# Optimization experiments

Measured on AMD Instinct MI355X. Metric: run time of the kernel, lower is better.

## Reference

```python
import math
import jax, jax.numpy as jnp
import numpy as np

NUM_EXPERTS = 64
HIDDEN = 2048
BATCH, SEQ = 8, 2048


def setup_inputs() -> dict:
    key = jax.random.key(0)
    k1, k2 = jax.random.split(key)
    hidden_states = jax.random.normal(k1, (BATCH, SEQ, HIDDEN), dtype=jnp.float32)
    classifier_weight = jax.random.normal(k2, (HIDDEN, NUM_EXPERTS), dtype=jnp.float32) * (1.0 / math.sqrt(HIDDEN))
    return {"hidden_states": hidden_states, "classifier_weight": classifier_weight}


def _route_tokens(router_logits):
    # router_logits: (tokens, experts). second_expert_policy='all',
    # normalize_router_prob_before_dropping=False, batch_prioritized_routing=True,
    # training mode -> capacity = 2*ceil(tokens/experts), no padding mask.
    n_tokens, n_experts = router_logits.shape
    router_probs = jax.nn.softmax(router_logits, axis=-1)  # router_dtype=float32

    top_1_idx = jnp.argmax(router_probs, axis=-1)
    top_1_mask = jax.nn.one_hot(top_1_idx, n_experts, dtype=router_probs.dtype)
    logits_except_top_1 = jnp.where(top_1_mask > 0, -jnp.inf, router_logits)
    top_2_idx = jnp.argmax(logits_except_top_1, axis=-1)
    top_2_mask = jax.nn.one_hot(top_2_idx, n_experts, dtype=router_probs.dtype)

    # batch-prioritized routing: sort tokens by -max prob, cumsum positions per expert
    importance = -jnp.max(router_probs, axis=-1)  # (tokens,)
    order = jnp.argsort(importance)
    inv_order = jnp.argsort(order)
    sorted_1 = top_1_mask[order]
    locations1 = ((jnp.cumsum(sorted_1, axis=0) - 1.0) * sorted_1)[inv_order]
    sorted_2 = top_2_mask[order]
    locations2 = ((jnp.cumsum(sorted_2, axis=0) - 1.0) * sorted_2)[inv_order]
    locations2 = locations2 + jnp.sum(top_1_mask, axis=0, keepdims=True)

    expert_capacity = 2 * math.ceil(n_tokens / n_experts)  # training path, expert_capacity=None
    top_1_mask = top_1_mask * (locations1 < expert_capacity).astype(top_1_mask.dtype)
    top_2_mask = top_2_mask * (locations2 < expert_capacity).astype(top_2_mask.dtype)

    # normalize AFTER dropping (normalize_router_prob_before_dropping=False)
    top_1_max_probs = jnp.sum(router_probs * top_1_mask, axis=-1)
    top_2_max_probs = jnp.sum(router_probs * top_2_mask, axis=-1)
    denom = jnp.clip(top_1_max_probs + top_2_max_probs, jnp.finfo(router_probs.dtype).eps, None)
    gates1 = (top_1_max_probs / denom)[:, None] * top_1_mask
    gates2 = (top_2_max_probs / denom)[:, None] * top_2_mask
    return top_1_mask, gates1 + gates2


def reference(hidden_states, classifier_weight):
    b, s, h = hidden_states.shape
    x = hidden_states.reshape(b * s, h)
    router_logits = x @ classifier_weight  # (tokens, experts), bias=False
    top_1_mask, router_probs = _route_tokens(router_logits)
    return top_1_mask, router_probs
```

## Files before the change

kernel.cpp:

```cpp
#include <hip/hip_runtime.h>
#include <math.h>

#define TOKENS      16384
#define HID         2048
#define EXPERTS     64
#define CAPSLOT     1024
#define CAP         512

__device__ __forceinline__ void fma8(float* a, float s, float4 w0, float4 w1) {
    a[0] = fmaf(s, w0.x, a[0]); a[1] = fmaf(s, w0.y, a[1]);
    a[2] = fmaf(s, w0.z, a[2]); a[3] = fmaf(s, w0.w, a[3]);
    a[4] = fmaf(s, w1.x, a[4]); a[5] = fmaf(s, w1.y, a[5]);
    a[6] = fmaf(s, w1.z, a[6]); a[7] = fmaf(s, w1.w, a[7]);
}

template<int KCH>
__global__ __launch_bounds__(256) void k_partial(
    const float* __restrict__ x, const float* __restrict__ W,
    float* __restrict__ partial, int* __restrict__ cnts)
{
    __shared__ float wl[KCH * EXPERTS];

    const int tid = threadIdx.x;
    const int tb = blockIdx.x & 63;
    const int kc = blockIdx.x >> 6;
    const int k0 = kc * KCH;

    if (blockIdx.x == 0) {
        for (int i = tid; i < 128 * 16; i += 256) cnts[i] = 0;
    }

    {
        const float4* src = (const float4*)(W + (size_t)k0 * EXPERTS);
        float4* dst = (float4*)wl;
        #pragma unroll
        for (int i = 0; i < (KCH * EXPERTS / 4) / 256; ++i)
            dst[i * 256 + tid] = src[i * 256 + tid];
    }
    __syncthreads();

    const int lane = tid & 63;
    const int wv   = tid >> 6;
    const int tg   = lane >> 3;
    const int eg   = lane & 7;
    const int tok0 = tb * 256 + wv * 64 + tg * 8;
    const float* xb = x + (size_t)tok0 * HID + k0;

    float acc[8][8];
    #pragma unroll
    for (int i = 0; i < 8; ++i)
        #pragma unroll
        for (int e = 0; e < 8; ++e) acc[i][e] = 0.f;

    float4 xv[8];
    #pragma unroll
    for (int i = 0; i < 8; ++i)
        xv[i] = *(const float4*)(xb + (size_t)i * HID);

    #pragma unroll 2
    for (int k4 = 0; k4 < KCH; k4 += 4) {
        float4 xn[8];
        const bool more = (k4 + 4 < KCH);
        if (more) {
            #pragma unroll
            for (int i = 0; i < 8; ++i)
                xn[i] = *(const float4*)(xb + (size_t)i * HID + k4 + 4);
        }

        float4 w0[4], w1[4];
        #pragma unroll
        for (int kk = 0; kk < 4; ++kk) {
            const float* wp = &wl[(k4 + kk) * EXPERTS + eg * 8];
            w0[kk] = *(const float4*)wp;
            w1[kk] = *(const float4*)(wp + 4);
        }

        #pragma unroll
        for (int i = 0; i < 8; ++i) {
            fma8(acc[i], xv[i].x, w0[0], w1[0]);
            fma8(acc[i], xv[i].y, w0[1], w1[1]);
            fma8(acc[i], xv[i].z, w0[2], w1[2]);
            fma8(acc[i], xv[i].w, w0[3], w1[3]);
        }

        if (more) {
            #pragma unroll
            for (int i = 0; i < 8; ++i) xv[i] = xn[i];
        }
    }

    float* pb = partial + ((size_t)kc * TOKENS + tok0) * EXPERTS + eg * 8;
    #pragma unroll
    for (int i = 0; i < 8; ++i) {
        *(float4*)(pb + (size_t)i * EXPERTS) =
            make_float4(acc[i][0], acc[i][1], acc[i][2], acc[i][3]);
        *(float4*)(pb + (size_t)i * EXPERTS + 4) =
            make_float4(acc[i][4], acc[i][5], acc[i][6], acc[i][7]);
    }
}

template<int KSPLIT>
__global__ __launch_bounds__(256) void k_route(
    const float* __restrict__ partial,
    float* __restrict__ p1o, float* __restrict__ p2o,
    int* __restrict__ top1o, int* __restrict__ top2o,
    int* __restrict__ cnts, float* __restrict__ bkey, int* __restrict__ btok)
{
    const int tid   = threadIdx.x;
    const int e     = tid & 63;
    const int token = blockIdx.x * 4 + (tid >> 6);

    float logit = 0.f;
    #pragma unroll
    for (int c = 0; c < KSPLIT; ++c)
        logit += partial[((size_t)c * TOKENS + token) * EXPERTS + e];

    float bv = logit; int be = e;
    #pragma unroll
    for (int m = 32; m >= 1; m >>= 1) {
        float ov = __shfl_xor(bv, m);
        int   oe = __shfl_xor(be, m);
        if (ov > bv || (ov == bv && oe < be)) { bv = ov; be = oe; }
    }
    const float m1 = bv;
    const int   e1 = be;

    float bv2 = (e == e1) ? -INFINITY : logit;
    int   be2 = (e == e1) ? (1 << 30) : e;
    #pragma unroll
    for (int m = 32; m >= 1; m >>= 1) {
        float ov = __shfl_xor(bv2, m);
        int   oe = __shfl_xor(be2, m);
        if (ov > bv2 || (ov == bv2 && oe < be2)) { bv2 = ov; be2 = oe; }
    }
    const int e2 = be2;

    float s = expf(logit - m1);
    #pragma unroll
    for (int m = 32; m >= 1; m >>= 1) s += __shfl_xor(s, m);

    if (e == 0) {
        const float P1 = 1.0f / s;
        p1o[token]   = P1;
        p2o[token]   = expf(bv2 - m1) / s;
        top1o[token] = e1;
        top2o[token] = e2;

        int s1 = atomicAdd(&cnts[e1 * 16], 1);
        if (s1 < CAPSLOT) {
            bkey[(size_t)e1 * CAPSLOT + s1] = P1;
            btok[(size_t)e1 * CAPSLOT + s1] = token;
        }
        int s2 = atomicAdd(&cnts[(64 + e2) * 16], 1);
        if (s2 < CAPSLOT) {
            bkey[(size_t)(64 + e2) * CAPSLOT + s2] = P1;
            btok[(size_t)(64 + e2) * CAPSLOT + s2] = token;
        }
    }
}

__global__ __launch_bounds__(256) void k_rank(
    const int* __restrict__ cnts,
    const float* __restrict__ bkey, const int* __restrict__ btok,
    int* __restrict__ keep1, int* __restrict__ keep2)
{
    __shared__ float skey[CAPSLOT];
    __shared__ int   stok[CAPSLOT];

    const int b    = blockIdx.x;
    const int mode = b >> 6;
    const int e    = b & 63;
    const int tid  = threadIdx.x;

    const int n_raw = cnts[b * 16];
    const int n     = min(n_raw, CAPSLOT);
    const int base  = mode ? cnts[e * 16] : 0;

    for (int i = tid; i < n; i += 256) {
        skey[i] = bkey[(size_t)b * CAPSLOT + i];
        stok[i] = btok[(size_t)b * CAPSLOT + i];
    }
    __syncthreads();

    int* __restrict__ keep = mode ? keep2 : keep1;
    for (int i = tid; i < n; i += 256) {
        const float ki = skey[i];
        const int   ti = stok[i];
        int r = base;
        for (int j = 0; j < n; ++j)
            r += (skey[j] > ki || (skey[j] == ki && stok[j] < ti)) ? 1 : 0;
        keep[ti] = (r < CAP) ? 1 : 0;
    }
}

__global__ __launch_bounds__(256) void k_out(
    const float* __restrict__ p1, const float* __restrict__ p2,
    const int* __restrict__ top1, const int* __restrict__ top2,
    const int* __restrict__ keep1, const int* __restrict__ keep2,
    float* __restrict__ out)
{
    const int tid   = threadIdx.x;
    const int token = blockIdx.x * 16 + (tid >> 4);
    const int eb    = (tid & 15) * 4;

    const int  k1 = keep1[token];
    const int  k2 = keep2[token];
    const float P1 = k1 ? p1[token] : 0.0f;
    const float P2 = k2 ? p2[token] : 0.0f;
    const float denom = fmaxf(P1 + P2, 1.1920929e-07f);
    const float g1 = P1 / denom;
    const float g2 = P2 / denom;
    const int e1 = top1[token];
    const int e2 = top2[token];

    float4 mv, pv;
    mv.x = (k1 && e1 == eb + 0) ? 1.0f : 0.0f;
    mv.y = (k1 && e1 == eb + 1) ? 1.0f : 0.0f;
    mv.z = (k1 && e1 == eb + 2) ? 1.0f : 0.0f;
    mv.w = (k1 && e1 == eb + 3) ? 1.0f : 0.0f;
    pv.x = (k1 && e1 == eb + 0) ? g1 : ((k2 && e2 == eb + 0) ? g2 : 0.0f);
    pv.y = (k1 && e1 == eb + 1) ? g1 : ((k2 && e2 == eb + 1) ? g2 : 0.0f);
    pv.z = (k1 && e1 == eb + 2) ? g1 : ((k2 && e2 == eb + 2) ? g2 : 0.0f);
    pv.w = (k1 && e1 == eb + 3) ? g1 : ((k2 && e2 == eb + 3) ? g2 : 0.0f);

    *(float4*)(out + (size_t)token * EXPERTS + eb) = mv;
    *(float4*)(out + (size_t)TOKENS * EXPERTS + (size_t)token * EXPERTS + eb) = pv;
}

extern "C" void kernel_launch(void* const* d_in, const int* in_sizes, int n_in,
                              void* d_out, int out_size, void* d_ws, size_t ws_size,
                              hipStream_t stream)
{
    const float* x = (const float*)d_in[0];
    const float* W = (const float*)d_in[1];
    float* out = (float*)d_out;

    const size_t extras_f = 6 * (size_t)TOKENS
                          + 128 * 16
                          + 2 * 128 * (size_t)CAPSLOT;
    const size_t need8 = ((size_t)8 * TOKENS * EXPERTS + extras_f) * 4;
    const bool big = (ws_size == 0) || (ws_size >= need8);
    const int  ks  = big ? 8 : 4;

    float* partial = (float*)d_ws;
    float* p1    = partial + (size_t)ks * TOKENS * EXPERTS;
    float* p2    = p1 + TOKENS;
    int*   top1  = (int*)(p2 + TOKENS);
    int*   top2  = top1 + TOKENS;
    int*   keep1 = top2 + TOKENS;
    int*   keep2 = keep1 + TOKENS;
    int*   cnts  = keep2 + TOKENS;
    float* bkey  = (float*)(cnts + 128 * 16);
    int*   btok  = (int*)(bkey + 128 * CAPSLOT);

    if (big) {
        k_partial<256><<<64 * 8, 256, 0, stream>>>(x, W, partial, cnts);
        k_route<8><<<TOKENS / 4, 256, 0, stream>>>(
            partial, p1, p2, top1, top2, cnts, bkey, btok);
    } else {
        k_partial<512><<<64 * 4, 256, 0, stream>>>(x, W, partial, cnts);
        k_route<4><<<TOKENS / 4, 256, 0, stream>>>(
            partial, p1, p2, top1, top2, cnts, bkey, btok);
    }
    k_rank<<<2 * EXPERTS, 256, 0, stream>>>(cnts, bkey, btok, keep1, keep2);
    k_out<<<TOKENS / 16, 256, 0, stream>>>(
        p1, p2, top1, top2, keep1, keep2, out);
}
```

Baseline: 258.4 us.

## Add 16-way K-split GEMM with 16-token-per-thread register tiles

```diff
diff --git a/kernel.cpp b/kernel.cpp
--- a/kernel.cpp
+++ b/kernel.cpp
@@ -14,8 +14,79 @@
     a[6] = fmaf(s, w1.z, a[6]); a[7] = fmaf(s, w1.w, a[7]);
 }
 
+__global__ __launch_bounds__(256, 2) void k_partial16(
+    const float* __restrict__ x, const float* __restrict__ W,
+    float* __restrict__ partial, int* __restrict__ cnts)
+{
+    __shared__ float wl[128 * EXPERTS];
+
+    const int tid = threadIdx.x;
+    const int tb = blockIdx.x & 31;
+    const int kc = blockIdx.x >> 5;
+    const int k0 = kc * 128;
+
+    if (blockIdx.x == 0) {
+        for (int i = tid; i < 128 * 16; i += 256) cnts[i] = 0;
+    }
+
+    {
+        const float4* src = (const float4*)(W + (size_t)k0 * EXPERTS);
+        float4* dst = (float4*)wl;
+        #pragma unroll
+        for (int i = 0; i < 8; ++i)
+            dst[i * 256 + tid] = src[i * 256 + tid];
+    }
+    __syncthreads();
+
+    const int lane = tid & 63;
+    const int wv   = tid >> 6;
+    const int tg   = lane >> 3;
+    const int eg   = lane & 7;
+    const int tok0 = tb * 512 + wv * 128 + tg * 16;
+    const float* xb = x + (size_t)tok0 * HID + k0;
+
+    float acc[16][8];
+    #pragma unroll
+    for (int i = 0; i < 16; ++i)
+        #pragma unroll
+        for (int e = 0; e < 8; ++e) acc[i][e] = 0.f;
+
+    #pragma unroll 1
+    for (int k4 = 0; k4 < 128; k4 += 4) {
+        float4 xv[16];
+        #pragma unroll
+        for (int i = 0; i < 16; ++i)
+            xv[i] = *(const float4*)(xb + (size_t)i * HID + k4);
+
+        float4 w0[4], w1[4];
+        #pragma unroll
+        for (int kk = 0; kk < 4; ++kk) {
+            const float* wp = &wl[(k4 + kk) * EXPERTS + eg * 8];
+            w0[kk] = *(const float4*)wp;
+            w1[kk] = *(const float4*)(wp + 4);
+        }
+
+        #pragma unroll
+        for (int i = 0; i < 16; ++i) {
+            fma8(acc[i], xv[i].x, w0[0], w1[0]);
+            fma8(acc[i], xv[i].y, w0[1], w1[1]);
+            fma8(acc[i], xv[i].z, w0[2], w1[2]);
+            fma8(acc[i], xv[i].w, w0[3], w1[3]);
+        }
+    }
+
+    float* pb = partial + ((size_t)kc * TOKENS + tok0) * EXPERTS + eg * 8;
+    #pragma unroll
+    for (int i = 0; i < 16; ++i) {
+        *(float4*)(pb + (size_t)i * EXPERTS) =
+            make_float4(acc[i][0], acc[i][1], acc[i][2], acc[i][3]);
+        *(float4*)(pb + (size_t)i * EXPERTS + 4) =
+            make_float4(acc[i][4], acc[i][5], acc[i][6], acc[i][7]);
+    }
+}
+
 template<int KCH>
-__global__ __launch_bounds__(256) void k_partial(
+__global__ __launch_bounds__(256) void k_partial8(
     const float* __restrict__ x, const float* __restrict__ W,
     float* __restrict__ partial, int* __restrict__ cnts)
 {
@@ -235,12 +306,15 @@
     const float* W = (const float*)d_in[1];
     float* out = (float*)d_out;
 
-    const size_t extras_f = 6 * (size_t)TOKENS
-                          + 128 * 16
+    const size_t extras_f = 6 * (size_t)TOKENS + 128 * 16
                           + 2 * 128 * (size_t)CAPSLOT;
-    const size_t need8 = ((size_t)8 * TOKENS * EXPERTS + extras_f) * 4;
-    const bool big = (ws_size == 0) || (ws_size >= need8);
-    const int  ks  = big ? 8 : 4;
+    const size_t need16 = ((size_t)16 * TOKENS * EXPERTS + extras_f) * 4;
+    const size_t need8  = ((size_t)8  * TOKENS * EXPERTS + extras_f) * 4;
+
+    int ks;
+    if (ws_size == 0 || ws_size >= need16) ks = 16;
+    else if (ws_size >= need8)             ks = 8;
+    else                                   ks = 4;
 
     float* partial = (float*)d_ws;
     float* p1    = partial + (size_t)ks * TOKENS * EXPERTS;
@@ -253,12 +327,16 @@
     float* bkey  = (float*)(cnts + 128 * 16);
     int*   btok  = (int*)(bkey + 128 * CAPSLOT);
 
-    if (big) {
-        k_partial<256><<<64 * 8, 256, 0, stream>>>(x, W, partial, cnts);
+    if (ks == 16) {
+        k_partial16<<<32 * 16, 256, 0, stream>>>(x, W, partial, cnts);
+        k_route<16><<<TOKENS / 4, 256, 0, stream>>>(
+            partial, p1, p2, top1, top2, cnts, bkey, btok);
+    } else if (ks == 8) {
+        k_partial8<256><<<64 * 8, 256, 0, stream>>>(x, W, partial, cnts);
         k_route<8><<<TOKENS / 4, 256, 0, stream>>>(
             partial, p1, p2, top1, top2, cnts, bkey, btok);
     } else {
-        k_partial<512><<<64 * 4, 256, 0, stream>>>(x, W, partial, cnts);
+        k_partial8<512><<<64 * 4, 256, 0, stream>>>(x, W, partial, cnts);
         k_route<4><<<TOKENS / 4, 256, 0, stream>>>(
             partial, p1, p2, top1, top2, cnts, bkey, btok);
     }
```

Measured after the change: 281.8 us. 1.09x slower.
